# Kernel optimization log

Measured on AMD Instinct MI355X. Metric: run time of the kernel, lower is better.

The kernel has to match this reference:

```python
import jax, jax.numpy as jnp
import numpy as np

N_E, E_DIM = 1024, 256

def setup_inputs() -> dict:
    key = jax.random.key(0)
    k1, k2 = jax.random.split(key)
    z = jax.random.normal(k1, (16, E_DIM, 64, 64), dtype=jnp.float32)
    codebook = jax.random.normal(k2, (N_E, E_DIM), dtype=jnp.float32)
    return {"z": z, "codebook": codebook}

def reference(z, codebook):
    B, C, H, W = z.shape  # C == e_dim
    zp = jnp.transpose(z, (0, 2, 3, 1))          # B,H,W,C
    zf = zp.reshape(-1, C)                        # N,C with N=B*H*W
    # L2 distance: ||z||^2 + ||c||^2 - 2 z c^T  -> [N, n_e]
    d = (jnp.sum(zf * zf, axis=1, keepdims=True)
         + jnp.sum(codebook * codebook, axis=1)
         - 2.0 * jnp.matmul(zf, codebook.T))
    idx = jnp.argmin(d, axis=1)                   # [N] int
    # one-hot @ codebook == gather (same math)
    z_q = codebook[idx].reshape(zp.shape)         # B,H,W,C
    codebook_loss = jnp.mean((z_q - jax.lax.stop_gradient(zp)) ** 2)
    z_q_out = jnp.transpose(z_q, (0, 3, 1, 2))    # B,C,H,W
    min_encoding_indices = idx.reshape(B, 1, H, W)
    return (z_q_out, codebook_loss, jnp.zeros((), z_q_out.dtype), min_encoding_indices)
```

## Files before the change

kernel.cpp:

```cpp
#include <hip/hip_runtime.h>

#define HW 4096
#define NE 1024
#define LOSS_OFF 16777216
#define IDX_OFF  16777218
#define MARGIN 0.08f

typedef __attribute__((ext_vector_type(8))) _Float16 half8v;
typedef __attribute__((ext_vector_type(4))) float float4v;

#define WS_LIST_OFF   64
#define WS_CNORM_OFF  262208
#define WS_CBH_OFF    266304
#define WS_PART_OFF   790592

__device__ __forceinline__ unsigned short f16rne(float f) {
    _Float16 h = (_Float16)f;
    return __builtin_bit_cast(unsigned short, h);
}

__device__ __forceinline__ unsigned f16pk(float a, float b) {
    auto h = __builtin_amdgcn_cvt_pkrtz(a, b);
    return __builtin_bit_cast(unsigned, h);
}

__device__ __forceinline__ void stage16(const void* g, void* l) {
    __builtin_amdgcn_global_load_lds(
        (const __attribute__((address_space(1))) unsigned*)g,
        (__attribute__((address_space(3))) unsigned*)l, 16, 0, 0);
}

__global__ __launch_bounds__(256) void k0_prep(const float* __restrict__ cb,
                                               float* __restrict__ cnorm,
                                               unsigned short* __restrict__ cbh,
                                               int* __restrict__ flagcnt) {
    int e = blockIdx.x * 256 + threadIdx.x;
    if (e == 0) *flagcnt = 0;
    const float4* row = (const float4*)(cb + (size_t)e * 256);
    unsigned short* dst = cbh + (size_t)e * 256;
    float s = 0.f;
#pragma unroll 8
    for (int i = 0; i < 64; ++i) {
        float4 v = row[i];
        s += v.x * v.x + v.y * v.y + v.z * v.z + v.w * v.w;
        unsigned p0 = (unsigned)f16rne(v.x) | ((unsigned)f16rne(v.y) << 16);
        unsigned p1 = (unsigned)f16rne(v.z) | ((unsigned)f16rne(v.w) << 16);
        *(uint2*)(dst + i * 4) = make_uint2(p0, p1);
    }
    cnorm[e] = 0.5f * s;
}

__global__ __launch_bounds__(256, 3) void k1_mfma(const float* __restrict__ z,
                                                  const unsigned short* __restrict__ cbh,
                                                  const float* __restrict__ cnorm,
                                                  float* __restrict__ out_idx,
                                                  int* __restrict__ flagcnt,
                                                  int* __restrict__ flaglist) {
    __shared__ __align__(16) char smem[34304];
    char* bufs = smem;
    float* cand1 = (float*)(smem + 32768);
    int*   candi = (int*)  (smem + 33280);
    float* cand2 = (float*)(smem + 33792);

    const int tid = threadIdx.x;
    const int lane = tid & 63, w = tid >> 6;
    const int wx = w & 1, wy = w >> 1;
    const int lr = lane & 15, lg = lane >> 4;
    const unsigned bswz = (unsigned)(lr << 4);

    const int n0 = blockIdx.x * 64;
    const int hw0 = n0 & 4095;
    const float* zb = z + (size_t)(n0 >> 12) * (256 * HW);
    const char* cbh_b = (const char*)cbh;

    {
        const int row = tid & 63, kg8 = tid >> 6;
        const unsigned zswz = (unsigned)((row & 15) << 4);
#pragma unroll
        for (int it = 0; it < 8; ++it) {
            int kb = (kg8 + it * 4) * 8;
            float v[8];
#pragma unroll
            for (int q = 0; q < 8; ++q) v[q] = zb[(size_t)(kb + q) * HW + hw0 + row];
            unsigned pk[4];
#pragma unroll
            for (int q = 0; q < 4; ++q) pk[q] = f16pk(v[2*q], v[2*q+1]);
            unsigned scol = (unsigned)(kb * 2) ^ zswz;
            *(int4*)(smem + row * 512 + scol) = make_int4(pk[0], pk[1], pk[2], pk[3]);
        }
    }
    __syncthreads();

    half8v A[2][8];
#pragma unroll
    for (int mi = 0; mi < 2; ++mi)
#pragma unroll
        for (int ks = 0; ks < 8; ++ks)
            A[mi][ks] = *(const half8v*)(smem + (32*wy + 16*mi + lr) * 512
                                              + ((unsigned)(64*ks + 16*lg) ^ bswz));
    __syncthreads();

    const int i0 = w * 4;
    const int elo_half = lane >> 5;
    const unsigned col0 = (unsigned)((lane & 31) * 16);

#pragma unroll
    for (int i = 0; i < 4; ++i) {
        int e_loc = 2 * (i0 + i) + elo_half;
        unsigned col = col0 ^ (unsigned)((e_loc & 15) << 4);
        stage16(cbh_b + (size_t)e_loc * 512 + col, bufs + (i0 + i) * 1024);
    }
    __syncthreads();

    const float* cnp = cnorm + 16 * wx + lr;
    float b1[8], b2[8]; int bi[8];
#pragma unroll
    for (int i = 0; i < 8; ++i) { b1[i] = 1e30f; b2[i] = 1e30f; bi[i] = 0; }

    for (int c = 0; c < 32; ++c) {
        if (c < 31) {
            char* nb = bufs + ((c + 1) & 1) * 16384;
            const size_t ebase = (size_t)(c + 1) * 32;
#pragma unroll
            for (int i = 0; i < 4; ++i) {
                int e_loc = 2 * (i0 + i) + elo_half;
                unsigned col = col0 ^ (unsigned)((e_loc & 15) << 4);
                stage16(cbh_b + (ebase + e_loc) * 512 + col, nb + (i0 + i) * 1024);
            }
        }

        const char* bp = bufs + (c & 1) * 16384 + (16 * wx + lr) * 512;
        float4v a0 = {0.f,0.f,0.f,0.f}, a1 = a0;
#pragma unroll
        for (int ks = 0; ks < 8; ++ks) {
            half8v B = *(const half8v*)(bp + ((unsigned)(64*ks + 16*lg) ^ bswz));
            a0 = __builtin_amdgcn_mfma_f32_16x16x32_f16(A[0][ks], B, a0, 0, 0, 0);
            a1 = __builtin_amdgcn_mfma_f32_16x16x32_f16(A[1][ks], B, a1, 0, 0, 0);
        }

        const float cn = cnp[c * 32];
        const int e = c * 32 + 16 * wx + lr;
#pragma unroll
        for (int r = 0; r < 4; ++r) {
            float s0 = cn - a0[r];
            b2[r] = fminf(b2[r], fmaxf(b1[r], s0));
            if (s0 < b1[r]) { b1[r] = s0; bi[r] = e; }
            float s1 = cn - a1[r];
            b2[4+r] = fminf(b2[4+r], fmaxf(b1[4+r], s1));
            if (s1 < b1[4+r]) { b1[4+r] = s1; bi[4+r] = e; }
        }

        __syncthreads();
    }

#pragma unroll
    for (int m = 1; m <= 8; m <<= 1) {
#pragma unroll
        for (int s = 0; s < 8; ++s) {
            float o1 = __shfl_xor(b1[s], m, 64);
            float o2 = __shfl_xor(b2[s], m, 64);
            int   oi = __shfl_xor(bi[s], m, 64);
            float m2 = fminf(fmaxf(b1[s], o1), fminf(b2[s], o2));
            if (o1 < b1[s] || (o1 == b1[s] && oi < bi[s])) { b1[s] = o1; bi[s] = oi; }
            b2[s] = m2;
        }
    }
    if (lr == 0) {
#pragma unroll
        for (int mi = 0; mi < 2; ++mi)
#pragma unroll
            for (int r = 0; r < 4; ++r) {
                int row = 32 * wy + 16 * mi + 4 * lg + r;
                cand1[row * 2 + wx] = b1[mi * 4 + r];
                cand2[row * 2 + wx] = b2[mi * 4 + r];
                candi[row * 2 + wx] = bi[mi * 4 + r];
            }
    }
    __syncthreads();
    if (tid < 64) {
        float s1a = cand1[tid * 2], s1b = cand1[tid * 2 + 1];
        int   ia = candi[tid * 2],  ib = candi[tid * 2 + 1];
        float s2 = fminf(fminf(cand2[tid * 2], cand2[tid * 2 + 1]), fmaxf(s1a, s1b));
        float s1; int iw;
        if (s1b < s1a || (s1b == s1a && ib < ia)) { s1 = s1b; iw = ib; }
        else { s1 = s1a; iw = ia; }
        out_idx[n0 + tid] = (float)iw;
        if (s2 - s1 < MARGIN) {
            int p = atomicAdd(flagcnt, 1);
            flaglist[p] = n0 + tid;
        }
    }
}

__global__ __launch_bounds__(256) void k1b_refine(const float* __restrict__ z,
                                                  const float* __restrict__ cb,
                                                  const float* __restrict__ cnorm,
                                                  const int* __restrict__ flagcnt,
                                                  const int* __restrict__ flaglist,
                                                  float* __restrict__ out_idx) {
    __shared__ float zr[4][260];
    __shared__ int   rows[4];
    __shared__ float wb[4][4];
    __shared__ int   wi[4][4];
    const int tid = threadIdx.x;
    const int lane = tid & 63, w = tid >> 6;
    const int gid = tid >> 2, j = tid & 3;
    const int count = *flagcnt;
    for (int base = blockIdx.x * 4; base < count; base += gridDim.x * 4) {
        const int nr = min(4, count - base);
        __syncthreads();
        if (tid < nr) rows[tid] = flaglist[base + tid];
        __syncthreads();
        for (int r = 0; r < nr; ++r) {
            const int n = rows[r];
            zr[r][tid] = z[((size_t)(n >> 12) * 256 + tid) * HW + (n & 4095)];
        }
        __syncthreads();

        float acc[16][4];
#pragma unroll
        for (int p = 0; p < 16; ++p)
#pragma unroll
            for (int r = 0; r < 4; ++r) acc[p][r] = 0.f;

        const char* cbase = (const char*)cb + (size_t)gid * 1024 + j * 16;
#pragma unroll 2
        for (int q = 0; q < 16; ++q) {
            float4 zv[4];
#pragma unroll
            for (int r = 0; r < 4; ++r) zv[r] = *(const float4*)(&zr[r][q * 16 + j * 4]);
#pragma unroll
            for (int p = 0; p < 16; ++p) {
                float4 c = *(const float4*)(cbase + (size_t)p * 65536 + q * 64);
#pragma unroll
                for (int r = 0; r < 4; ++r) {
                    float a = acc[p][r];
                    a = fmaf(zv[r].x, c.x, a);
                    a = fmaf(zv[r].y, c.y, a);
                    a = fmaf(zv[r].z, c.z, a);
                    a = fmaf(zv[r].w, c.w, a);
                    acc[p][r] = a;
                }
            }
        }

        float best[4]; int bidx[4];
#pragma unroll
        for (int r = 0; r < 4; ++r) { best[r] = 1e30f; bidx[r] = 0; }
#pragma unroll
        for (int p = 0; p < 16; ++p) {
            const int e = p * 64 + gid;
            const float cn = cnorm[e];
#pragma unroll
            for (int r = 0; r < 4; ++r) {
                float d = acc[p][r];
                d += __shfl_xor(d, 1, 64);
                d += __shfl_xor(d, 2, 64);
                float s = cn - d;
                if (s < best[r]) { best[r] = s; bidx[r] = e; }
            }
        }
#pragma unroll
        for (int m = 1; m <= 32; m <<= 1) {
#pragma unroll
            for (int r = 0; r < 4; ++r) {
                float ob = __shfl_xor(best[r], m, 64);
                int   oi = __shfl_xor(bidx[r], m, 64);
                if (ob < best[r] || (ob == best[r] && oi < bidx[r])) { best[r] = ob; bidx[r] = oi; }
            }
        }
        if (lane == 0) {
#pragma unroll
            for (int r = 0; r < 4; ++r) { wb[w][r] = best[r]; wi[w][r] = bidx[r]; }
        }
        __syncthreads();
        if (tid < nr) {
            float bb = wb[0][tid]; int ii = wi[0][tid];
#pragma unroll
            for (int q = 1; q < 4; ++q)
                if (wb[q][tid] < bb || (wb[q][tid] == bb && wi[q][tid] < ii)) { bb = wb[q][tid]; ii = wi[q][tid]; }
            out_idx[rows[tid]] = (float)ii;
        }
        __syncthreads();
    }
}

__global__ __launch_bounds__(256) void k2_scatter(const float* __restrict__ z,
                                                  const float* __restrict__ cb,
                                                  const float* __restrict__ idxf,
                                                  float* __restrict__ zq,
                                                  float* __restrict__ part) {
    __shared__ float cbrow[64][257];
    __shared__ int   earr[64];
    __shared__ float ls[4];
    const int tid = threadIdx.x;
    const int b = blockIdx.x >> 6;
    const int hw0 = (blockIdx.x & 63) * 64;

    if (tid < 64) earr[tid] = (int)idxf[b * 4096 + hw0 + tid];
    __syncthreads();
    {
        const int r = tid >> 2, qd = tid & 3;
        const float4* src = (const float4*)(cb + (size_t)earr[r] * 256 + qd * 64);
#pragma unroll
        for (int i = 0; i < 16; ++i) {
            float4 v = src[i];
            float* d = &cbrow[r][qd * 64 + i * 4];
            d[0] = v.x; d[1] = v.y; d[2] = v.z; d[3] = v.w;
        }
    }
    __syncthreads();

    const int hw = tid & 63, cq = tid >> 6;
    const size_t zbase = ((size_t)b * 256) * 4096 + hw0 + hw;
    float lsum = 0.f;
#pragma unroll 8
    for (int pass = 0; pass < 64; ++pass) {
        const int c = pass * 4 + cq;
        const size_t flat = zbase + (size_t)c * 4096;
        float q = cbrow[hw][c];
        zq[flat] = q;
        float d = q - z[flat];
        lsum = fmaf(d, d, lsum);
    }
#pragma unroll
    for (int m = 32; m >= 1; m >>= 1) lsum += __shfl_down(lsum, m, 64);
    const int lane = tid & 63, w = tid >> 6;
    if (lane == 0) ls[w] = lsum;
    __syncthreads();
    if (tid == 0) part[blockIdx.x] = ls[0] + ls[1] + ls[2] + ls[3];
}

__global__ __launch_bounds__(256) void k3_final(const float* __restrict__ part,
                                                float* __restrict__ dout) {
    __shared__ float ls[4];
    float s = 0.f;
#pragma unroll
    for (int it = 0; it < 4; ++it) s += part[threadIdx.x + it * 256];
#pragma unroll
    for (int m = 32; m >= 1; m >>= 1) s += __shfl_down(s, m, 64);
    int lane = threadIdx.x & 63, w = threadIdx.x >> 6;
    if (lane == 0) ls[w] = s;
    __syncthreads();
    if (threadIdx.x == 0) {
        float total = ls[0] + ls[1] + ls[2] + ls[3];
        dout[LOSS_OFF]     = total / 16777216.0f;
        dout[LOSS_OFF + 1] = 0.0f;
    }
}

extern "C" void kernel_launch(void* const* d_in, const int* in_sizes, int n_in,
                              void* d_out, int out_size, void* d_ws, size_t ws_size,
                              hipStream_t stream) {
    const float* z  = (const float*)d_in[0];
    const float* cb = (const float*)d_in[1];
    float* out = (float*)d_out;
    char* ws = (char*)d_ws;

    int*            flagcnt  = (int*)ws;
    int*            flaglist = (int*)(ws + WS_LIST_OFF);
    float*          cnorm    = (float*)(ws + WS_CNORM_OFF);
    unsigned short* cbh      = (unsigned short*)(ws + WS_CBH_OFF);
    float*          part     = (float*)(ws + WS_PART_OFF);

    hipLaunchKernelGGL(k0_prep,   dim3(4),    dim3(256), 0, stream, cb, cnorm, cbh, flagcnt);
    hipLaunchKernelGGL(k1_mfma,   dim3(1024), dim3(256), 0, stream,
                       z, cbh, cnorm, out + IDX_OFF, flagcnt, flaglist);
    hipLaunchKernelGGL(k1b_refine, dim3(2048), dim3(256), 0, stream,
                       z, cb, cnorm, flagcnt, flaglist, out + IDX_OFF);
    hipLaunchKernelGGL(k2_scatter, dim3(1024), dim3(256), 0, stream,
                       z, cb, out + IDX_OFF, out, part);
    hipLaunchKernelGGL(k3_final,  dim3(1),    dim3(256), 0, stream, part, out);
}
```

Measured before the change: 144.6 us.

## Give each wave a private codebook stream and drop per-chunk block barriers

The main distance kernel now has each wave stage its own half of the codebook (512 entries, 16 per step) into a private double buffer. It waits on its own loads with explicit vmcnt waits instead of a block-wide __syncthreads every chunk. This removes 32 barriers per block and lets waves run out of lockstep. The cost is doubled shared memory (about 67KB), no explicit occupancy hint, and each wave now loads its codebook half independently, which raises global/L2 traffic. The prep kernel also splits each codebook row across 4 threads with shuffle reduction, using 16 blocks instead of 4.

```diff
diff --git a/kernel.cpp b/kernel.cpp
--- a/kernel.cpp
+++ b/kernel.cpp
@@ -34,39 +34,41 @@
                                                float* __restrict__ cnorm,
                                                unsigned short* __restrict__ cbh,
                                                int* __restrict__ flagcnt) {
-    int e = blockIdx.x * 256 + threadIdx.x;
-    if (e == 0) *flagcnt = 0;
-    const float4* row = (const float4*)(cb + (size_t)e * 256);
-    unsigned short* dst = cbh + (size_t)e * 256;
+    const int tid = threadIdx.x;
+    if (blockIdx.x == 0 && tid == 0) *flagcnt = 0;
+    const int e = blockIdx.x * 64 + (tid >> 2);
+    const int j = tid & 3;
+    const float4* src = (const float4*)(cb + (size_t)e * 256 + j * 64);
+    unsigned short* dst = cbh + (size_t)e * 256 + j * 64;
     float s = 0.f;
-#pragma unroll 8
-    for (int i = 0; i < 64; ++i) {
-        float4 v = row[i];
+#pragma unroll
+    for (int i = 0; i < 16; ++i) {
+        float4 v = src[i];
         s += v.x * v.x + v.y * v.y + v.z * v.z + v.w * v.w;
         unsigned p0 = (unsigned)f16rne(v.x) | ((unsigned)f16rne(v.y) << 16);
         unsigned p1 = (unsigned)f16rne(v.z) | ((unsigned)f16rne(v.w) << 16);
         *(uint2*)(dst + i * 4) = make_uint2(p0, p1);
     }
-    cnorm[e] = 0.5f * s;
-}
-
-__global__ __launch_bounds__(256, 3) void k1_mfma(const float* __restrict__ z,
-                                                  const unsigned short* __restrict__ cbh,
-                                                  const float* __restrict__ cnorm,
-                                                  float* __restrict__ out_idx,
-                                                  int* __restrict__ flagcnt,
-                                                  int* __restrict__ flaglist) {
-    __shared__ __align__(16) char smem[34304];
-    char* bufs = smem;
-    float* cand1 = (float*)(smem + 32768);
-    int*   candi = (int*)  (smem + 33280);
-    float* cand2 = (float*)(smem + 33792);
+    s += __shfl_xor(s, 1, 64);
+    s += __shfl_xor(s, 2, 64);
+    if (j == 0) cnorm[e] = 0.5f * s;
+}
+
+__global__ __launch_bounds__(256) void k1_mfma(const float* __restrict__ z,
+                                               const unsigned short* __restrict__ cbh,
+                                               const float* __restrict__ cnorm,
+                                               float* __restrict__ out_idx,
+                                               int* __restrict__ flagcnt,
+                                               int* __restrict__ flaglist) {
+    __shared__ __align__(16) char smem[67072];
+    float* cand1 = (float*)(smem + 65536);
+    int*   candi = (int*)  (smem + 66048);
+    float* cand2 = (float*)(smem + 66560);
 
     const int tid = threadIdx.x;
-    const int lane = tid & 63, w = tid >> 6;
-    const int wx = w & 1, wy = w >> 1;
+    const int lane = tid & 63, wid = tid >> 6;
+    const int wx = wid & 1, wy = wid >> 1;
     const int lr = lane & 15, lg = lane >> 4;
-    const unsigned bswz = (unsigned)(lr << 4);
 
     const int n0 = blockIdx.x * 64;
     const int hw0 = n0 & 4095;
@@ -97,49 +99,55 @@
 #pragma unroll
         for (int ks = 0; ks < 8; ++ks)
             A[mi][ks] = *(const half8v*)(smem + (32*wy + 16*mi + lr) * 512
-                                              + ((unsigned)(64*ks + 16*lg) ^ bswz));
-    __syncthreads();
-
-    const int i0 = w * 4;
-    const int elo_half = lane >> 5;
-    const unsigned col0 = (unsigned)((lane & 31) * 16);
-
-#pragma unroll
-    for (int i = 0; i < 4; ++i) {
-        int e_loc = 2 * (i0 + i) + elo_half;
-        unsigned col = col0 ^ (unsigned)((e_loc & 15) << 4);
-        stage16(cbh_b + (size_t)e_loc * 512 + col, bufs + (i0 + i) * 1024);
-    }
-    __syncthreads();
-
-    const float* cnp = cnorm + 16 * wx + lr;
+                                              + ((unsigned)(64*ks + 16*lg) ^ (unsigned)(lr << 4)));
+    __syncthreads();
+
+    char* mybuf0 = smem + wid * 8192;
+    char* mybuf1 = smem + 32768 + wid * 8192;
+    const int el      = (lane >> 5);
+    const unsigned c0 = (unsigned)((lane & 31) * 16);
+    const size_t  eb0 = (size_t)wx * 512;
+
+#pragma unroll
+    for (int i = 0; i < 8; ++i) {
+        int e_loc = 2 * i + el;
+        unsigned col = c0 ^ (unsigned)((e_loc & 15) << 4);
+        stage16(cbh_b + (eb0 + e_loc) * 512 + col, mybuf0 + i * 1024);
+    }
+
+    const float* cnp = cnorm + wx * 512 + lr;
     float b1[8], b2[8]; int bi[8];
 #pragma unroll
     for (int i = 0; i < 8; ++i) { b1[i] = 1e30f; b2[i] = 1e30f; bi[i] = 0; }
 
     for (int c = 0; c < 32; ++c) {
+        char* cur = (c & 1) ? mybuf1 : mybuf0;
         if (c < 31) {
-            char* nb = bufs + ((c + 1) & 1) * 16384;
-            const size_t ebase = (size_t)(c + 1) * 32;
-#pragma unroll
-            for (int i = 0; i < 4; ++i) {
-                int e_loc = 2 * (i0 + i) + elo_half;
-                unsigned col = col0 ^ (unsigned)((e_loc & 15) << 4);
-                stage16(cbh_b + (ebase + e_loc) * 512 + col, nb + (i0 + i) * 1024);
-            }
-        }
-
-        const char* bp = bufs + (c & 1) * 16384 + (16 * wx + lr) * 512;
+            char* nb = (c & 1) ? mybuf0 : mybuf1;
+            const size_t ebase = eb0 + (size_t)(c + 1) * 16;
+#pragma unroll
+            for (int i = 0; i < 8; ++i) {
+                int e_loc = 2 * i + el;
+                unsigned col = c0 ^ (unsigned)((e_loc & 15) << 4);
+                stage16(cbh_b + (ebase + e_loc) * 512 + col, nb + i * 1024);
+            }
+            asm volatile("s_waitcnt vmcnt(8)" ::: "memory");
+        } else {
+            asm volatile("s_waitcnt vmcnt(0)" ::: "memory");
+        }
+        __builtin_amdgcn_sched_barrier(0);
+
+        const char* bp = cur + lr * 512;
         float4v a0 = {0.f,0.f,0.f,0.f}, a1 = a0;
 #pragma unroll
         for (int ks = 0; ks < 8; ++ks) {
-            half8v B = *(const half8v*)(bp + ((unsigned)(64*ks + 16*lg) ^ bswz));
+            half8v B = *(const half8v*)(bp + ((unsigned)(64*ks + 16*lg) ^ (unsigned)(lr << 4)));
             a0 = __builtin_amdgcn_mfma_f32_16x16x32_f16(A[0][ks], B, a0, 0, 0, 0);
             a1 = __builtin_amdgcn_mfma_f32_16x16x32_f16(A[1][ks], B, a1, 0, 0, 0);
         }
 
-        const float cn = cnp[c * 32];
-        const int e = c * 32 + 16 * wx + lr;
+        const float cn = cnp[c * 16];
+        const int e = wx * 512 + c * 16 + lr;
 #pragma unroll
         for (int r = 0; r < 4; ++r) {
             float s0 = cn - a0[r];
@@ -149,8 +157,6 @@
             b2[4+r] = fminf(b2[4+r], fmaxf(b1[4+r], s1));
             if (s1 < b1[4+r]) { b1[4+r] = s1; bi[4+r] = e; }
         }
-
-        __syncthreads();
     }
 
 #pragma unroll
@@ -363,7 +369,7 @@
     unsigned short* cbh      = (unsigned short*)(ws + WS_CBH_OFF);
     float*          part     = (float*)(ws + WS_PART_OFF);
 
-    hipLaunchKernelGGL(k0_prep,   dim3(4),    dim3(256), 0, stream, cb, cnorm, cbh, flagcnt);
+    hipLaunchKernelGGL(k0_prep,   dim3(16),   dim3(256), 0, stream, cb, cnorm, cbh, flagcnt);
     hipLaunchKernelGGL(k1_mfma,   dim3(1024), dim3(256), 0, stream,
                        z, cbh, cnorm, out + IDX_OFF, flagcnt, flaglist);
     hipLaunchKernelGGL(k1b_refine, dim3(2048), dim3(256), 0, stream,
```

Result: faster. 135.6 us (-6.2%).
